# Optimization experiments

Hardware: AMD Instinct MI355X
Metric: run time of the kernel (lower is better)

Reference implementation:

```python
import jax, jax.numpy as jnp
import numpy as np

BLOCK = 64          # block_dim
GAPS = (1, 64)      # block_dim**i for i in range(num_layers=2), input_dim=4096
N_BLOCKS = 64       # input_dim // block_dim
HID = 128           # 2 * block_dim (hidden_layers_ratio=[2])
BS = 8192
IN_DIM = 4096


def setup_inputs() -> dict:
    key = jax.random.key(0)
    kx, kw1, kw2 = jax.random.split(key, 3)
    x = jax.random.normal(kx, (BS, IN_DIM), dtype=jnp.float32)
    # one BlockResMLP per factorized layer: BlockLinear(64, 64, 128) -> ELU -> BlockLinear(64, 128, 64)
    w1 = jax.random.normal(kw1, (len(GAPS), N_BLOCKS, BLOCK, HID), dtype=jnp.float32) / np.sqrt(BLOCK)
    b1 = jnp.zeros((len(GAPS), N_BLOCKS, 1, HID), dtype=jnp.float32)
    w2 = jax.random.normal(kw2, (len(GAPS), N_BLOCKS, HID, BLOCK), dtype=jnp.float32) / np.sqrt(HID)
    b2 = jnp.zeros((len(GAPS), N_BLOCKS, 1, BLOCK), dtype=jnp.float32)
    return {"x": x, "w1": w1, "b1": b1, "w2": w2, "b2": b2}


def _facto(y, w1, b1, w2, b2):
    # BlockResMLP.forward: view(bs, n_blocks, BLOCK).transpose(0,1) -> batched block GEMMs -> residual
    bs = y.shape[0]
    z = y.reshape(bs, -1, BLOCK).transpose(1, 0, 2)              # (n_blocks, bs, BLOCK)
    h = jnp.einsum('nbd,nde->nbe', z, w1) + b1                   # BlockLinear 1 + bias
    h = jax.nn.elu(h)                                            # ELU (alpha=1)
    h = jnp.einsum('nbe,ned->nbd', h, w2) + b2                   # BlockLinear 2 + bias
    z = h + z                                                    # residual
    return z.transpose(1, 0, 2).reshape(bs, -1)


def reference(x, w1, b1, w2, b2):
    bs = x.shape[0]
    y = x
    for i, gap in enumerate(GAPS):
        # permutation shuffle: view(-1, BLOCK, gap).transpose(2,1).contiguous().view(bs,-1)
        y = y.reshape(-1, BLOCK, gap).transpose(0, 2, 1).reshape(bs, -1)
        y = _facto(y, w1[i], b1[i], w2[i], b2[i])
        # inverse shuffle: view(-1, gap, BLOCK).transpose(2,1)
        y = y.reshape(-1, gap, BLOCK).transpose(0, 2, 1).reshape(bs, -1)
    return y
```

## Files before the change

### kernel.cpp

```cpp
#include <hip/hip_runtime.h>


typedef short short8 __attribute__((ext_vector_type(8)));
typedef float floatx4 __attribute__((ext_vector_type(4)));

#define MFMA(A, B, C) __builtin_amdgcn_mfma_f32_16x16x32_bf16((A), (B), (C), 0, 0, 0)

__device__ __forceinline__ unsigned short bf16r(float f) {
  unsigned int u = __builtin_bit_cast(unsigned int, f);
  u += 0x7FFFu + ((u >> 16) & 1u);
  return (unsigned short)(u >> 16);
}
__device__ __forceinline__ float bf16f(unsigned short h) {
  unsigned int u = ((unsigned int)h) << 16;
  return __builtin_bit_cast(float, u);
}
__device__ __forceinline__ float eluf(float v) {
  return v > 0.f ? v : (__expf(v) - 1.f);
}
__device__ __forceinline__ uint4 gather8(const short* base, int stride) {
  uint4 o;
  o.x = (unsigned int)(unsigned short)base[0 * stride] |
        ((unsigned int)(unsigned short)base[1 * stride] << 16);
  o.y = (unsigned int)(unsigned short)base[2 * stride] |
        ((unsigned int)(unsigned short)base[3 * stride] << 16);
  o.z = (unsigned int)(unsigned short)base[4 * stride] |
        ((unsigned int)(unsigned short)base[5 * stride] << 16);
  o.w = (unsigned int)(unsigned short)base[6 * stride] |
        ((unsigned int)(unsigned short)base[7 * stride] << 16);
  return o;
}

__global__ __launch_bounds__(256) void k0_prep(const float* __restrict__ w1,
                                               const float* __restrict__ w2,
                                               short* __restrict__ w1t,
                                               short* __restrict__ w2t) {
  __shared__ __align__(16) short T[128 * 72];
  const int t  = threadIdx.x;
  const int ln = blockIdx.x >> 1;
  if ((blockIdx.x & 1) == 0) {
    const float* src = w1 + (size_t)ln * 8192 + t * 32;
    const int d = t >> 2, e0 = (t & 3) * 32;
#pragma unroll
    for (int u = 0; u < 32; u += 2) {
      float f0 = src[u], f1 = src[u + 1];
      unsigned int pk = (unsigned int)bf16r(f0) | ((unsigned int)bf16r(f1) << 16);
      *(unsigned int*)&T[d * 136 + e0 + u] = pk;
    }
    __syncthreads();
    const int e = t >> 1, d0 = (t & 1) * 32;
    short* dst = w1t + (size_t)ln * 8192 + e * 64 + d0;
#pragma unroll
    for (int k = 0; k < 4; ++k)
      *(uint4*)(dst + k * 8) = gather8(&T[(d0 + k * 8) * 136 + e], 136);
  } else {
    const float* src = w2 + (size_t)ln * 8192 + t * 32;
    const int e = t >> 1, d0 = (t & 1) * 32;
#pragma unroll
    for (int u = 0; u < 32; u += 2) {
      float f0 = src[u], f1 = src[u + 1];
      unsigned int pk = (unsigned int)bf16r(f0) | ((unsigned int)bf16r(f1) << 16);
      *(unsigned int*)&T[e * 72 + d0 + u] = pk;
    }
    __syncthreads();
    const int dp = t >> 2, e0 = (t & 3) * 32;
    short* dst = w2t + (size_t)ln * 8192 + dp * 128 + e0;
#pragma unroll
    for (int k = 0; k < 4; ++k)
      *(uint4*)(dst + k * 8) = gather8(&T[(e0 + k * 8) * 72 + dp], 72);
  }
}

__global__ __launch_bounds__(256) void k1_layer0(
    const float* __restrict__ x,
    const short* __restrict__ w1t, const short* __restrict__ w2t,
    const float* __restrict__ b1,  const float* __restrict__ b2,
    short* __restrict__ y1) {
  __shared__ __align__(16) short hst[4][2][16][72];
  const int tid  = threadIdx.x;
  const int lane = tid & 63;
  const int wv   = tid >> 6;
  const int il   = lane & 15;
  const int q    = lane >> 4;
  const int npair   = blockIdx.x & 31;
  const int rowtile = blockIdx.x >> 5;
  const int n  = npair * 2 + (wv & 1);
  const int r0 = rowtile * 64 + (wv >> 1) * 32;

  const short* w1n = w1t + (size_t)n * 8192;
  const short* w2n = w2t + (size_t)n * 8192;
  const float* b1n = b1 + n * 128;
  const float* b2n = b2 + n * 64;

  short8 a[2][2];
#pragma unroll
  for (int Mt = 0; Mt < 2; ++Mt) {
#pragma unroll
    for (int ks = 0; ks < 2; ++ks) {
      const float* xp = x + (size_t)(r0 + Mt * 16 + il) * 4096 + n * 64 + ks * 32 + q * 8;
      floatx4 f0 = *(const floatx4*)xp;
      floatx4 f1 = *(const floatx4*)(xp + 4);
      short8 t;
#pragma unroll
      for (int u = 0; u < 4; ++u) { t[u] = (short)bf16r(f0[u]); t[4 + u] = (short)bf16r(f1[u]); }
      a[ks][Mt] = t;
    }
  }

  floatx4 acc2[2][4] = {};
  for (int hh = 0; hh < 2; ++hh) {
    floatx4 acc1[2][4] = {};
#pragma unroll
    for (int ks = 0; ks < 2; ++ks) {
#pragma unroll
      for (int nt = 0; nt < 4; ++nt) {
        short8 b = *(const short8*)(w1n + (hh * 64 + nt * 16 + il) * 64 + ks * 32 + q * 8);
        acc1[0][nt] = MFMA(a[ks][0], b, acc1[0][nt]);
        acc1[1][nt] = MFMA(a[ks][1], b, acc1[1][nt]);
      }
    }
#pragma unroll
    for (int nt = 0; nt < 4; ++nt) {
      float bias = b1n[hh * 64 + nt * 16 + il];
#pragma unroll
      for (int Mt = 0; Mt < 2; ++Mt)
#pragma unroll
        for (int rg = 0; rg < 4; ++rg) {
          float v = acc1[Mt][nt][rg] + bias;
          hst[wv][Mt][q * 4 + rg][nt * 16 + il] = (short)bf16r(eluf(v));
        }
    }
    asm volatile("s_waitcnt lgkmcnt(0)" ::: "memory");
#pragma unroll
    for (int ks2 = 0; ks2 < 2; ++ks2) {
      short8 a2[2];
      a2[0] = *(const short8*)&hst[wv][0][il][ks2 * 32 + q * 8];
      a2[1] = *(const short8*)&hst[wv][1][il][ks2 * 32 + q * 8];
#pragma unroll
      for (int nt2 = 0; nt2 < 4; ++nt2) {
        short8 b = *(const short8*)(w2n + (nt2 * 16 + il) * 128 + hh * 64 + ks2 * 32 + q * 8);
        acc2[0][nt2] = MFMA(a2[0], b, acc2[0][nt2]);
        acc2[1][nt2] = MFMA(a2[1], b, acc2[1][nt2]);
      }
    }
    asm volatile("s_waitcnt lgkmcnt(0)" ::: "memory");
  }
#pragma unroll
  for (int Mt = 0; Mt < 2; ++Mt) {
    const int R0 = r0 + Mt * 16 + q * 4;
    const size_t nbase = ((size_t)((r0 + Mt * 16) >> 4) * 64 + n) * 64;
#pragma unroll
    for (int nt2 = 0; nt2 < 4; ++nt2) {
      const int j = nt2 * 16 + il;
      const float bias = b2n[j];
      float v0 = acc2[Mt][nt2][0] + bias + x[(size_t)(R0 + 0) * 4096 + n * 64 + j];
      float v1 = acc2[Mt][nt2][1] + bias + x[(size_t)(R0 + 1) * 4096 + n * 64 + j];
      float v2 = acc2[Mt][nt2][2] + bias + x[(size_t)(R0 + 2) * 4096 + n * 64 + j];
      float v3 = acc2[Mt][nt2][3] + bias + x[(size_t)(R0 + 3) * 4096 + n * 64 + j];
      uint2 pk;
      pk.x = (unsigned int)bf16r(v0) | ((unsigned int)bf16r(v1) << 16);
      pk.y = (unsigned int)bf16r(v2) | ((unsigned int)bf16r(v3) << 16);
      *(uint2*)(y1 + (nbase + j) * 16 + q * 4) = pk;
    }
  }
}

__global__ __launch_bounds__(256) void k2_layer1_out(
    const short* __restrict__ y1,
    const short* __restrict__ w1t, const short* __restrict__ w2t,
    const float* __restrict__ b1,  const float* __restrict__ b2,
    float* __restrict__ out) {
  __shared__ __align__(16) short zL2[16 * 1160];
  __shared__ __align__(16) short hs[4][16][72];
  const int tid  = threadIdx.x;
  const int lane = tid & 63;
  const int wv   = tid >> 6;
  const int il   = lane & 15;
  const int q    = lane >> 4;
  const int rt16 = blockIdx.x & 511;
  const int m0   = (blockIdx.x >> 9) * 16;

  {
    const int i   = tid >> 2;
    const int sub = tid & 3;
    const short* src = y1 + ((size_t)(rt16 * 64 + i) * 64 + m0 + sub * 4) * 16;
#pragma unroll
    for (int j = 0; j < 8; ++j) {
      uint4 w = *(const uint4*)(src + j * 8);
      const int mm = j >> 1;
      const int rb = (j & 1) * 8;
      unsigned int c[4] = {w.x, w.y, w.z, w.w};
      short* zb = zL2 + (sub * 4 + mm) * 1160 + i;
#pragma unroll
      for (int h = 0; h < 4; ++h) {
        zb[(rb + h * 2 + 0) * 72] = (short)(c[h] & 0xffffu);
        zb[(rb + h * 2 + 1) * 72] = (short)(c[h] >> 16);
      }
    }
  }
  __syncthreads();

#pragma unroll
  for (int mi = 0; mi < 4; ++mi) {
    const int ml = wv * 4 + mi;
    const int m  = m0 + ml;
    const short* w1m = w1t + (size_t)(64 + m) * 8192;
    const short* w2m = w2t + (size_t)(64 + m) * 8192;
    const float* b1m = b1 + (64 + m) * 128;
    const float* b2m = b2 + (64 + m) * 64;
    short* zrow = zL2 + ml * 1160;

    floatx4 acc2[4] = {};
    for (int hh = 0; hh < 2; ++hh) {
      floatx4 acc1[4] = {};
#pragma unroll
      for (int ks = 0; ks < 2; ++ks) {
        short8 a = *(const short8*)(zrow + il * 72 + ks * 32 + q * 8);
#pragma unroll
        for (int nt = 0; nt < 4; ++nt) {
          short8 b = *(const short8*)(w1m + (hh * 64 + nt * 16 + il) * 64 + ks * 32 + q * 8);
          acc1[nt] = MFMA(a, b, acc1[nt]);
        }
      }
#pragma unroll
      for (int nt = 0; nt < 4; ++nt) {
        float bias = b1m[hh * 64 + nt * 16 + il];
#pragma unroll
        for (int rg = 0; rg < 4; ++rg)
          hs[wv][q * 4 + rg][nt * 16 + il] = (short)bf16r(eluf(acc1[nt][rg] + bias));
      }
      asm volatile("s_waitcnt lgkmcnt(0)" ::: "memory");
#pragma unroll
      for (int ks2 = 0; ks2 < 2; ++ks2) {
        short8 a2 = *(const short8*)&hs[wv][il][ks2 * 32 + q * 8];
#pragma unroll
        for (int nt2 = 0; nt2 < 4; ++nt2) {
          short8 b = *(const short8*)(w2m + (nt2 * 16 + il) * 128 + hh * 64 + ks2 * 32 + q * 8);
          acc2[nt2] = MFMA(a2, b, acc2[nt2]);
        }
      }
      asm volatile("s_waitcnt lgkmcnt(0)" ::: "memory");
    }
#pragma unroll
    for (int nt2 = 0; nt2 < 4; ++nt2) {
      const int i = nt2 * 16 + il;
      const float bias = b2m[i];
#pragma unroll
      for (int k = 0; k < 4; ++k) {
        short* slot = zrow + (q * 4 + k) * 72 + i;
        float r = bf16f((unsigned short)*slot);
        *slot = (short)bf16r(acc2[nt2][k] + bias + r);
      }
    }
  }
  __syncthreads();

  const int r = tid >> 4;
  const int c = tid & 15;
  float* orow = out + (size_t)(rt16 * 16 + r) * 4096 + m0;
#pragma unroll
  for (int k = 0; k < 4; ++k) {
    const int i = c * 4 + k;
    float vv[16];
#pragma unroll
    for (int ml = 0; ml < 16; ++ml)
      vv[ml] = bf16f((unsigned short)zL2[ml * 1160 + r * 72 + i]);
    float* op = orow + i * 64;
    floatx4 a0 = {vv[0],  vv[1],  vv[2],  vv[3]};
    floatx4 a1 = {vv[4],  vv[5],  vv[6],  vv[7]};
    floatx4 a2 = {vv[8],  vv[9],  vv[10], vv[11]};
    floatx4 a3 = {vv[12], vv[13], vv[14], vv[15]};
    *(floatx4*)(op + 0)  = a0;
    *(floatx4*)(op + 4)  = a1;
    *(floatx4*)(op + 8)  = a2;
    *(floatx4*)(op + 12) = a3;
  }
}

extern "C" void kernel_launch(void* const* d_in, const int* in_sizes, int n_in,
                              void* d_out, int out_size, void* d_ws, size_t ws_size,
                              hipStream_t stream) {
  const float* x  = (const float*)d_in[0];
  const float* w1 = (const float*)d_in[1];
  const float* b1 = (const float*)d_in[2];
  const float* w2 = (const float*)d_in[3];
  const float* b2 = (const float*)d_in[4];
  float* out = (float*)d_out;

  short* w1t = (short*)d_ws;
  short* w2t = w1t + (1u << 20);
  short* y1  = w2t + (1u << 20);

  hipLaunchKernelGGL(k0_prep,       dim3(256),  dim3(256), 0, stream, w1, w2, w1t, w2t);
  hipLaunchKernelGGL(k1_layer0,     dim3(4096), dim3(256), 0, stream, x, w1t, w2t, b1, b2, y1);
  hipLaunchKernelGGL(k2_layer1_out, dim3(2048), dim3(256), 0, stream, y1, w1t, w2t, b1, b2, out);
}
```

Measured before the change: 453.8 us.

## Transpose fragments in registers via permutation MFMA instead of LDS staging in layer-1 kernel

The layer-1 kernel no longer stages the whole y1 tile in shared memory or round-trips the ELU hidden activations through LDS. Each wave loads its input fragments straight from global memory. It then moves the accumulator layout into MFMA operand layout by multiplying with a one-hot permutation matrix, and the layer-1 weights are pre-permuted in the prep kernel to match the new K ordering. The output staging buffer is re-laid out so the final store reads packed 32-bit LDS words. This removes LDS traffic, waitcnts and a barrier, at the cost of extra MFMA instructions and less coalesced global loads of y1.

```diff
diff --git a/kernel.cpp b/kernel.cpp
--- a/kernel.cpp
+++ b/kernel.cpp
@@ -2,7 +2,9 @@
 
 
 typedef short short8 __attribute__((ext_vector_type(8)));
+typedef short short4v __attribute__((ext_vector_type(4)));
 typedef float floatx4 __attribute__((ext_vector_type(4)));
+typedef unsigned int uintx4 __attribute__((ext_vector_type(4)));
 
 #define MFMA(A, B, C) __builtin_amdgcn_mfma_f32_16x16x32_bf16((A), (B), (C), 0, 0, 0)
 
@@ -15,19 +17,22 @@
   unsigned int u = ((unsigned int)h) << 16;
   return __builtin_bit_cast(float, u);
 }
+__device__ __forceinline__ unsigned int pk2(float lo, float hi) {
+  return (unsigned int)bf16r(lo) | ((unsigned int)bf16r(hi) << 16);
+}
 __device__ __forceinline__ float eluf(float v) {
   return v > 0.f ? v : (__expf(v) - 1.f);
 }
-__device__ __forceinline__ uint4 gather8(const short* base, int stride) {
+__device__ __forceinline__ uint4 gather44(const short* A, const short* B, int s) {
   uint4 o;
-  o.x = (unsigned int)(unsigned short)base[0 * stride] |
-        ((unsigned int)(unsigned short)base[1 * stride] << 16);
-  o.y = (unsigned int)(unsigned short)base[2 * stride] |
-        ((unsigned int)(unsigned short)base[3 * stride] << 16);
-  o.z = (unsigned int)(unsigned short)base[4 * stride] |
-        ((unsigned int)(unsigned short)base[5 * stride] << 16);
-  o.w = (unsigned int)(unsigned short)base[6 * stride] |
-        ((unsigned int)(unsigned short)base[7 * stride] << 16);
+  o.x = (unsigned int)(unsigned short)A[0 * s] |
+        ((unsigned int)(unsigned short)A[1 * s] << 16);
+  o.y = (unsigned int)(unsigned short)A[2 * s] |
+        ((unsigned int)(unsigned short)A[3 * s] << 16);
+  o.z = (unsigned int)(unsigned short)B[0 * s] |
+        ((unsigned int)(unsigned short)B[1 * s] << 16);
+  o.w = (unsigned int)(unsigned short)B[2 * s] |
+        ((unsigned int)(unsigned short)B[3 * s] << 16);
   return o;
 }
 
@@ -38,36 +43,39 @@
   __shared__ __align__(16) short T[128 * 72];
   const int t  = threadIdx.x;
   const int ln = blockIdx.x >> 1;
+  const bool pm = (ln >= 64);
   if ((blockIdx.x & 1) == 0) {
     const float* src = w1 + (size_t)ln * 8192 + t * 32;
     const int d = t >> 2, e0 = (t & 3) * 32;
 #pragma unroll
     for (int u = 0; u < 32; u += 2) {
-      float f0 = src[u], f1 = src[u + 1];
-      unsigned int pk = (unsigned int)bf16r(f0) | ((unsigned int)bf16r(f1) << 16);
-      *(unsigned int*)&T[d * 136 + e0 + u] = pk;
+      *(unsigned int*)&T[d * 136 + e0 + u] = pk2(src[u], src[u + 1]);
     }
     __syncthreads();
     const int e = t >> 1, d0 = (t & 1) * 32;
     short* dst = w1t + (size_t)ln * 8192 + e * 64 + d0;
 #pragma unroll
-    for (int k = 0; k < 4; ++k)
-      *(uint4*)(dst + k * 8) = gather8(&T[(d0 + k * 8) * 136 + e], 136);
+    for (int k = 0; k < 4; ++k) {
+      const int ta = d0 + (pm ? 4 * k : 8 * k);
+      const int tb = d0 + (pm ? 16 + 4 * k : 8 * k + 4);
+      *(uint4*)(dst + k * 8) = gather44(&T[ta * 136 + e], &T[tb * 136 + e], 136);
+    }
   } else {
     const float* src = w2 + (size_t)ln * 8192 + t * 32;
     const int e = t >> 1, d0 = (t & 1) * 32;
 #pragma unroll
     for (int u = 0; u < 32; u += 2) {
-      float f0 = src[u], f1 = src[u + 1];
-      unsigned int pk = (unsigned int)bf16r(f0) | ((unsigned int)bf16r(f1) << 16);
-      *(unsigned int*)&T[e * 72 + d0 + u] = pk;
+      *(unsigned int*)&T[e * 72 + d0 + u] = pk2(src[u], src[u + 1]);
     }
     __syncthreads();
     const int dp = t >> 2, e0 = (t & 3) * 32;
     short* dst = w2t + (size_t)ln * 8192 + dp * 128 + e0;
 #pragma unroll
-    for (int k = 0; k < 4; ++k)
-      *(uint4*)(dst + k * 8) = gather8(&T[(e0 + k * 8) * 72 + dp], 72);
+    for (int k = 0; k < 4; ++k) {
+      const int ta = e0 + (pm ? 4 * k : 8 * k);
+      const int tb = e0 + (pm ? 16 + 4 * k : 8 * k + 4);
+      *(uint4*)(dst + k * 8) = gather44(&T[ta * 72 + dp], &T[tb * 72 + dp], 72);
+    }
   }
 }
 
@@ -158,47 +166,33 @@
       float v2 = acc2[Mt][nt2][2] + bias + x[(size_t)(R0 + 2) * 4096 + n * 64 + j];
       float v3 = acc2[Mt][nt2][3] + bias + x[(size_t)(R0 + 3) * 4096 + n * 64 + j];
       uint2 pk;
-      pk.x = (unsigned int)bf16r(v0) | ((unsigned int)bf16r(v1) << 16);
-      pk.y = (unsigned int)bf16r(v2) | ((unsigned int)bf16r(v3) << 16);
+      pk.x = pk2(v0, v1);
+      pk.y = pk2(v2, v3);
       *(uint2*)(y1 + (nbase + j) * 16 + q * 4) = pk;
     }
   }
 }
 
+#define RSTR 1156
+#define ISTR 18
 __global__ __launch_bounds__(256) void k2_layer1_out(
     const short* __restrict__ y1,
     const short* __restrict__ w1t, const short* __restrict__ w2t,
     const float* __restrict__ b1,  const float* __restrict__ b2,
     float* __restrict__ out) {
-  __shared__ __align__(16) short zL2[16 * 1160];
-  __shared__ __align__(16) short hs[4][16][72];
+  __shared__ __align__(16) short yo[16 * RSTR];
   const int tid  = threadIdx.x;
   const int lane = tid & 63;
   const int wv   = tid >> 6;
   const int il   = lane & 15;
   const int q    = lane >> 4;
-  const int rt16 = blockIdx.x & 511;
+  const int G    = blockIdx.x & 511;
   const int m0   = (blockIdx.x >> 9) * 16;
 
-  {
-    const int i   = tid >> 2;
-    const int sub = tid & 3;
-    const short* src = y1 + ((size_t)(rt16 * 64 + i) * 64 + m0 + sub * 4) * 16;
-#pragma unroll
-    for (int j = 0; j < 8; ++j) {
-      uint4 w = *(const uint4*)(src + j * 8);
-      const int mm = j >> 1;
-      const int rb = (j & 1) * 8;
-      unsigned int c[4] = {w.x, w.y, w.z, w.w};
-      short* zb = zL2 + (sub * 4 + mm) * 1160 + i;
-#pragma unroll
-      for (int h = 0; h < 4; ++h) {
-        zb[(rb + h * 2 + 0) * 72] = (short)(c[h] & 0xffffu);
-        zb[(rb + h * 2 + 1) * 72] = (short)(c[h] >> 16);
-      }
-    }
-  }
-  __syncthreads();
+  short8 pb;
+#pragma unroll
+  for (int v = 0; v < 8; ++v) pb[v] = (v < 4 && il == q * 4 + v) ? (short)0x3F80 : (short)0;
+  const floatx4 zero4 = {0.f, 0.f, 0.f, 0.f};
 
 #pragma unroll
   for (int mi = 0; mi < 4; ++mi) {
@@ -208,72 +202,97 @@
     const short* w2m = w2t + (size_t)(64 + m) * 8192;
     const float* b1m = b1 + (64 + m) * 128;
     const float* b2m = b2 + (64 + m) * 64;
-    short* zrow = zL2 + ml * 1160;
+
+    short4v za[4];
+#pragma unroll
+    for (int nt = 0; nt < 4; ++nt)
+      za[nt] = *(const short4v*)(y1 + ((size_t)(G * 64 + nt * 16 + il) * 64 + m) * 16 + q * 4);
+
+    floatx4 zd[4];
+#pragma unroll
+    for (int nt = 0; nt < 4; ++nt) {
+      short8 az = {za[nt][0], za[nt][1], za[nt][2], za[nt][3], 0, 0, 0, 0};
+      zd[nt] = MFMA(az, pb, zero4);
+    }
+    short8 at[2];
+#pragma unroll
+    for (int ks = 0; ks < 2; ++ks) {
+      uintx4 w;
+      w[0] = pk2(zd[2 * ks][0], zd[2 * ks][1]);
+      w[1] = pk2(zd[2 * ks][2], zd[2 * ks][3]);
+      w[2] = pk2(zd[2 * ks + 1][0], zd[2 * ks + 1][1]);
+      w[3] = pk2(zd[2 * ks + 1][2], zd[2 * ks + 1][3]);
+      at[ks] = __builtin_bit_cast(short8, w);
+    }
 
     floatx4 acc2[4] = {};
+    uintx4 a2w[4];
+#pragma unroll
     for (int hh = 0; hh < 2; ++hh) {
       floatx4 acc1[4] = {};
 #pragma unroll
-      for (int ks = 0; ks < 2; ++ks) {
-        short8 a = *(const short8*)(zrow + il * 72 + ks * 32 + q * 8);
+      for (int ks = 0; ks < 2; ++ks)
 #pragma unroll
         for (int nt = 0; nt < 4; ++nt) {
           short8 b = *(const short8*)(w1m + (hh * 64 + nt * 16 + il) * 64 + ks * 32 + q * 8);
-          acc1[nt] = MFMA(a, b, acc1[nt]);
+          acc1[nt] = MFMA(at[ks], b, acc1[nt]);
         }
-      }
 #pragma unroll
       for (int nt = 0; nt < 4; ++nt) {
-        float bias = b1m[hh * 64 + nt * 16 + il];
-#pragma unroll
-        for (int rg = 0; rg < 4; ++rg)
-          hs[wv][q * 4 + rg][nt * 16 + il] = (short)bf16r(eluf(acc1[nt][rg] + bias));
-      }
-      asm volatile("s_waitcnt lgkmcnt(0)" ::: "memory");
-#pragma unroll
-      for (int ks2 = 0; ks2 < 2; ++ks2) {
-        short8 a2 = *(const short8*)&hs[wv][il][ks2 * 32 + q * 8];
-#pragma unroll
-        for (int nt2 = 0; nt2 < 4; ++nt2) {
-          short8 b = *(const short8*)(w2m + (nt2 * 16 + il) * 128 + hh * 64 + ks2 * 32 + q * 8);
-          acc2[nt2] = MFMA(a2, b, acc2[nt2]);
-        }
-      }
-      asm volatile("s_waitcnt lgkmcnt(0)" ::: "memory");
+        const float bias = b1m[hh * 64 + nt * 16 + il];
+        short8 ha = {(short)bf16r(eluf(acc1[nt][0] + bias)),
+                     (short)bf16r(eluf(acc1[nt][1] + bias)),
+                     (short)bf16r(eluf(acc1[nt][2] + bias)),
+                     (short)bf16r(eluf(acc1[nt][3] + bias)),
+                     0, 0, 0, 0};
+        floatx4 hd = MFMA(ha, pb, zero4);
+        const int ks2 = hh * 2 + (nt >> 1);
+        const int hf  = nt & 1;
+        a2w[ks2][hf * 2 + 0] = pk2(hd[0], hd[1]);
+        a2w[ks2][hf * 2 + 1] = pk2(hd[2], hd[3]);
+      }
+    }
+#pragma unroll
+    for (int ks2 = 0; ks2 < 4; ++ks2) {
+      short8 af = __builtin_bit_cast(short8, a2w[ks2]);
+#pragma unroll
+      for (int nt2 = 0; nt2 < 4; ++nt2) {
+        short8 b = *(const short8*)(w2m + (nt2 * 16 + il) * 128 + ks2 * 32 + q * 8);
+        acc2[nt2] = MFMA(af, b, acc2[nt2]);
+      }
     }
 #pragma unroll
     for (int nt2 = 0; nt2 < 4; ++nt2) {
       const int i = nt2 * 16 + il;
       const float bias = b2m[i];
 #pragma unroll
-      for (int k = 0; k < 4; ++k) {
-        short* slot = zrow + (q * 4 + k) * 72 + i;
-        float r = bf16f((unsigned short)*slot);
-        *slot = (short)bf16r(acc2[nt2][k] + bias + r);
+      for (int rg = 0; rg < 4; ++rg) {
+        float val = acc2[nt2][rg] + bias + bf16f((unsigned short)za[nt2][rg]);
+        yo[(q * 4 + rg) * RSTR + i * ISTR + ml] = (short)bf16r(val);
       }
     }
   }
   __syncthreads();
 
-  const int r = tid >> 4;
-  const int c = tid & 15;
-  float* orow = out + (size_t)(rt16 * 16 + r) * 4096 + m0;
+  const int r  = tid & 15;
+  const int i0 = (tid >> 4) * 4;
+  float* orow = out + (size_t)(G * 16 + r) * 4096 + m0;
 #pragma unroll
   for (int k = 0; k < 4; ++k) {
-    const int i = c * 4 + k;
-    float vv[16];
-#pragma unroll
-    for (int ml = 0; ml < 16; ++ml)
-      vv[ml] = bf16f((unsigned short)zL2[ml * 1160 + r * 72 + i]);
+    const int i = i0 + k;
+    const short* yr = &yo[r * RSTR + i * ISTR];
+    float f[16];
+#pragma unroll
+    for (int j = 0; j < 8; ++j) {
+      unsigned int w = *(const unsigned int*)(yr + 2 * j);
+      f[2 * j]     = bf16f((unsigned short)(w & 0xffffu));
+      f[2 * j + 1] = bf16f((unsigned short)(w >> 16));
+    }
     float* op = orow + i * 64;
-    floatx4 a0 = {vv[0],  vv[1],  vv[2],  vv[3]};
-    floatx4 a1 = {vv[4],  vv[5],  vv[6],  vv[7]};
-    floatx4 a2 = {vv[8],  vv[9],  vv[10], vv[11]};
-    floatx4 a3 = {vv[12], vv[13], vv[14], vv[15]};
-    *(floatx4*)(op + 0)  = a0;
-    *(floatx4*)(op + 4)  = a1;
-    *(floatx4*)(op + 8)  = a2;
-    *(floatx4*)(op + 12) = a3;
+    *(floatx4*)(op + 0)  = (floatx4){f[0],  f[1],  f[2],  f[3]};
+    *(floatx4*)(op + 4)  = (floatx4){f[4],  f[5],  f[6],  f[7]};
+    *(floatx4*)(op + 8)  = (floatx4){f[8],  f[9],  f[10], f[11]};
+    *(floatx4*)(op + 12) = (floatx4){f[12], f[13], f[14], f[15]};
   }
 }
 
```

After: 466.7 us. +2.8%, slower.
